# Kernel optimization log

Measured on AMD Instinct MI355X. Metric: run time of the kernel, lower is better.

The kernel has to match this reference:

```python
import jax, jax.numpy as jnp
import numpy as np

N = 100000   # nodes
E = 1600000  # directed edges (avg degree 16)
IN = 256     # input feature dim


def _gcn_norm(src, dst, n):
    # PyG gcn_norm with unit edge weights: deg computed on destination,
    # norm = deg^{-1/2}[src] * deg^{-1/2}[dst]
    deg = jax.ops.segment_sum(jnp.ones_like(dst, jnp.float32), dst, num_segments=n)
    dinv = jnp.where(deg > 0, jax.lax.rsqrt(deg), 0.0)
    return dinv[src] * dinv[dst]


def _gcn_conv(x, W, b, src, dst, norm, n):
    h = x @ W                          # [N, out] dense transform first (PyG order)
    msg = norm[:, None] * h[src]       # gather + scale  [E+N, out]
    agg = jax.ops.segment_sum(msg, dst, num_segments=n)  # scatter-add
    return agg + b


def setup_inputs() -> dict:
    key = jax.random.key(0)
    ks = jax.random.split(key, 5)
    x = jax.random.normal(ks[0], (N, IN), jnp.float32)
    edge_index = jax.random.randint(ks[1], (2, E), 0, N, dtype=jnp.int32)
    W1 = jax.random.normal(ks[2], (IN, 64), jnp.float32) * (1.0 / np.sqrt(IN))
    b1 = jnp.zeros((64,), jnp.float32)
    W2 = jax.random.normal(ks[3], (64, 32), jnp.float32) * (1.0 / np.sqrt(64))
    b2 = jnp.zeros((32,), jnp.float32)
    Wlin = jax.random.normal(ks[4], (32, 1), jnp.float32) * (1.0 / np.sqrt(32))
    blin = jnp.zeros((1,), jnp.float32)
    return {"x": x, "edge_index": edge_index, "W1": W1, "b1": b1,
            "W2": W2, "b2": b2, "Wlin": Wlin, "blin": blin}


def reference(x, edge_index, W1, b1, W2, b2, Wlin, blin):
    n = x.shape[0]
    loops = jnp.arange(n, dtype=edge_index.dtype)  # add self-loops (GCNConv default)
    src = jnp.concatenate([edge_index[0], loops])
    dst = jnp.concatenate([edge_index[1], loops])
    norm = _gcn_norm(src, dst, n)                  # same for both layers
    h = jax.nn.relu(_gcn_conv(x, W1, b1, src, dst, norm, n))
    h = jax.nn.relu(_gcn_conv(h, W2, b2, src, dst, norm, n))
    return h @ Wlin + blin
```

## Files before the change

### kernel.cpp

```cpp
#include <hip/hip_runtime.h>
#include <hip/hip_fp16.h>
#include <math.h>


#define BSH  9
#define BCAP 12288

typedef _Float16 half8 __attribute__((ext_vector_type(8)));
typedef _Float16 half4 __attribute__((ext_vector_type(4)));
typedef float floatx4 __attribute__((ext_vector_type(4)));

#define XT_STRIDE 40

static __global__ __launch_bounds__(256) void k_wfrag(const float* __restrict__ W1,
                                                      _Float16* __restrict__ w1f,
                                                      int* __restrict__ bkt_cnt) {
    int t = threadIdx.x;
    bkt_cnt[t] = 0;
    for (int idx = t; idx < 2048; idx += 256) {
        int kb = idx >> 8;
        int nt = (idx >> 6) & 3;
        int l  = idx & 63;
        int k0 = kb * 32 + ((l >> 4) << 3);
        int nn = nt * 16 + (l & 15);
        half8 b;
        #pragma unroll
        for (int j = 0; j < 8; ++j) b[j] = (_Float16)W1[(k0 + j) * 64 + nn];
        *(half8*)(w1f + (size_t)idx * 8) = b;
    }
}

static __global__ __launch_bounds__(256) void k_fat(const float* __restrict__ x,
                                                    const _Float16* __restrict__ w1f,
                                                    _Float16* __restrict__ h1f,
                                                    const int* __restrict__ src,
                                                    const int* __restrict__ dst,
                                                    int* __restrict__ bkt_cnt,
                                                    int* __restrict__ epack,
                                                    int n, int e, int nScat) {
    __shared__ alignas(16) char smem[32768 + 2 * 128 * XT_STRIDE * 2];
    int t = threadIdx.x;

    if ((int)blockIdx.x < nScat) {
        int*           sp    = (int*)smem;
        unsigned char* sbkt  = (unsigned char*)(smem + 16384);
        int*           cnt   = (int*)(smem + 20480);
        int*           loff  = (int*)(smem + 21504);
        int*           lcur  = (int*)(smem + 22528);
        int*           gbase = (int*)(smem + 23552);
        int*           sh    = (int*)(smem + 24576);
        int cb = blockIdx.x * 4096;
        int cc = min(4096, e - cb);

        cnt[t] = 0;
        __syncthreads();
        int ep[16]; unsigned char eb[16];
        int nv = 0;
        #pragma unroll
        for (int k = 0; k < 16; ++k) {
            int i = cb + k * 256 + t;
            if (i < e) {
                int s = src[i], d = dst[i];
                int b = d >> BSH;
                ep[nv] = ((d & 511) << 17) | s;
                eb[nv] = (unsigned char)b;
                atomicAdd(&cnt[b], 1);
                ++nv;
            }
        }
        __syncthreads();
        int v = cnt[t];
        sh[t] = v;
        __syncthreads();
        for (int o = 1; o < 256; o <<= 1) {
            int u = (t >= o) ? sh[t - o] : 0;
            __syncthreads();
            sh[t] += u;
            __syncthreads();
        }
        loff[t] = sh[t] - v;
        lcur[t] = sh[t] - v;
        if (v > 0) gbase[t] = t * BCAP + atomicAdd(&bkt_cnt[t], v);
        __syncthreads();
        for (int k = 0; k < nv; ++k) {
            int b = eb[k];
            int p = atomicAdd(&lcur[b], 1);
            sp[p] = ep[k];
            sbkt[p] = (unsigned char)b;
        }
        __syncthreads();
        for (int i = t; i < cc; i += 256) {
            int b = sbkt[i];
            epack[gbase[b] + (i - loff[b])] = sp[i];
        }
    } else {
        _Float16* Wl = (_Float16*)smem;
        _Float16* xt = (_Float16*)(smem + 32768);
        {
            const float4* s = (const float4*)w1f;
            float4* d = (float4*)smem;
            #pragma unroll
            for (int i = 0; i < 8; ++i) d[t + i * 256] = s[t + i * 256];
        }

        int l = t & 63;
        int w = t >> 6;
        int r0 = (blockIdx.x - nScat) * 128;
        int kq = (l >> 4) << 3;
        int lrow0 = w * 32 + (l & 15);
        int lrow1 = lrow0 + 16;

        int srow[4], sc4[4];
        const float* sgp[4];
        #pragma unroll
        for (int i = 0; i < 4; ++i) {
            int f = t + i * 256;
            srow[i] = f >> 3;
            sc4[i]  = f & 7;
            int gr  = r0 + srow[i];
            gr = gr < n ? gr : n - 1;
            sgp[i] = x + (size_t)gr * 256 + sc4[i] * 4;
        }

        floatx4 acc[2][4];
        #pragma unroll
        for (int mt = 0; mt < 2; ++mt)
            #pragma unroll
            for (int nt = 0; nt < 4; ++nt)
                acc[mt][nt] = (floatx4){0.f, 0.f, 0.f, 0.f};

        float4 pre[4];
        #pragma unroll
        for (int i = 0; i < 4; ++i) pre[i] = *(const float4*)(sgp[i]);
        #pragma unroll
        for (int i = 0; i < 4; ++i) {
            half4 h;
            h[0] = (_Float16)pre[i].x; h[1] = (_Float16)pre[i].y;
            h[2] = (_Float16)pre[i].z; h[3] = (_Float16)pre[i].w;
            *(half4*)(xt + srow[i] * XT_STRIDE + sc4[i] * 4) = h;
        }
        __syncthreads();

        #pragma unroll
        for (int kb = 0; kb < 8; ++kb) {
            if (kb < 7) {
                #pragma unroll
                for (int i = 0; i < 4; ++i)
                    pre[i] = *(const float4*)(sgp[i] + (kb + 1) * 32);
            }
            const _Float16* cur = xt + (kb & 1) * (128 * XT_STRIDE);
            half8 a0 = *(const half8*)(cur + lrow0 * XT_STRIDE + kq);
            half8 a1 = *(const half8*)(cur + lrow1 * XT_STRIDE + kq);
            #pragma unroll
            for (int nt = 0; nt < 4; ++nt) {
                half8 b = *(const half8*)(Wl + ((size_t)(kb * 4 + nt) * 64 + l) * 8);
                acc[0][nt] = __builtin_amdgcn_mfma_f32_16x16x32_f16(a0, b, acc[0][nt], 0, 0, 0);
                acc[1][nt] = __builtin_amdgcn_mfma_f32_16x16x32_f16(a1, b, acc[1][nt], 0, 0, 0);
            }
            if (kb < 7) {
                _Float16* nxt = xt + ((kb + 1) & 1) * (128 * XT_STRIDE);
                #pragma unroll
                for (int i = 0; i < 4; ++i) {
                    half4 h;
                    h[0] = (_Float16)pre[i].x; h[1] = (_Float16)pre[i].y;
                    h[2] = (_Float16)pre[i].z; h[3] = (_Float16)pre[i].w;
                    *(half4*)(nxt + srow[i] * XT_STRIDE + sc4[i] * 4) = h;
                }
                __syncthreads();
            }
        }

        int quad = l >> 4;
        int col  = l & 15;
        int rb0  = r0 + w * 32;
        #pragma unroll
        for (int mt = 0; mt < 2; ++mt) {
            #pragma unroll
            for (int r = 0; r < 4; ++r) {
                int rr = rb0 + mt * 16 + quad * 4 + r;
                if (rr < n) {
                    _Float16* o = h1f + (size_t)rr * 64 + col;
                    #pragma unroll
                    for (int nt = 0; nt < 4; ++nt)
                        o[nt * 16] = (_Float16)acc[mt][nt][r];
                }
            }
        }
    }
}

static __global__ __launch_bounds__(512) void k_bfinal(const int* __restrict__ bkt_cnt,
                                                       const int* __restrict__ epack,
                                                       float* __restrict__ dinv,
                                                       int* __restrict__ offs,
                                                       int* __restrict__ csr_src, int n) {
    __shared__ int cnt[512], sh[512], lcur[512];
    int t = threadIdx.x;
    int base = blockIdx.x << BSH;
    int e0 = blockIdx.x * BCAP;
    int e1 = e0 + bkt_cnt[blockIdx.x];
    cnt[t] = 0;
    __syncthreads();
    for (int i = e0 + t; i < e1; i += 512) atomicAdd(&cnt[epack[i] >> 17], 1);
    __syncthreads();
    int v = cnt[t];
    if (base + t < n) dinv[base + t] = 1.0f / sqrtf((float)(v + 1));
    sh[t] = v;
    __syncthreads();
    for (int o = 1; o < 512; o <<= 1) {
        int u = (t >= o) ? sh[t - o] : 0;
        __syncthreads();
        sh[t] += u;
        __syncthreads();
    }
    int incl = sh[t];
    if (base + t < n) offs[base + t] = e0 + incl;
    lcur[t] = e0 + incl - v;
    __syncthreads();
    for (int i = e0 + t; i < e1; i += 512) {
        int p = epack[i];
        int d = p >> 17;
        int pos = atomicAdd(&lcur[d], 1);
        csr_src[pos] = p & 0x1FFFF;
    }
}

static __global__ __launch_bounds__(512) void k_wpack(int* __restrict__ csr_src,
                                                      const float* __restrict__ dinv,
                                                      const int* __restrict__ bkt_cnt) {
    int b  = blockIdx.x;
    int e0 = b * BCAP;
    int e1 = e0 + bkt_cnt[b];
    for (int i = e0 + threadIdx.x; i < e1; i += 512) {
        int s = csr_src[i];
        int q = (int)(dinv[s] * 32767.0f + 0.5f);
        csr_src[i] = s | (q << 17);
    }
}

static __global__ __launch_bounds__(256) void k_agg1gemm2(const int* __restrict__ offs,
                                                          const int* __restrict__ csr_src,
                                                          const float* __restrict__ dinv,
                                                          const uint2* __restrict__ h1q,
                                                          const float* __restrict__ b1,
                                                          const float* __restrict__ W2,
                                                          __half2* __restrict__ h2h, int n) {
    __shared__ float Wl[64 * 32];
    __shared__ float aggL[16][64];
    int t = threadIdx.x;
    *(float4*)(Wl + t * 4)        = *(const float4*)(W2 + t * 4);
    *(float4*)(Wl + t * 4 + 1024) = *(const float4*)(W2 + t * 4 + 1024);

    int li = t & 15;
    int ni = t >> 4;
    int node  = blockIdx.x * 16 + ni;
    int nodeC = node < n ? node : n - 1;
    int start = (nodeC & 511) ? offs[nodeC - 1] : (nodeC >> BSH) * BCAP;
    int end   = offs[nodeC];
    float dd  = dinv[nodeC];

    uint2 su = h1q[(size_t)nodeC * 16 + li];
    float2 s01 = __half22float2(*(const __half2*)&su.x);
    float2 s23 = __half22float2(*(const __half2*)&su.y);
    float a0 = dd * s01.x, a1 = dd * s01.y, a2 = dd * s23.x, a3 = dd * s23.y;

    const float QS = 1.0f / 32767.0f;
    int j = start;
    for (; j + 7 < end; j += 8) {
        int pk[8];
        #pragma unroll
        for (int u = 0; u < 8; ++u) pk[u] = csr_src[j + u];
        uint2 vv[8]; float wq[8];
        #pragma unroll
        for (int u = 0; u < 8; ++u) {
            int s = pk[u] & 0x1FFFF;
            wq[u] = (float)(((unsigned)pk[u]) >> 17) * QS;
            vv[u] = h1q[(size_t)s * 16 + li];
        }
        #pragma unroll
        for (int u = 0; u < 8; ++u) {
            float2 v01 = __half22float2(*(const __half2*)&vv[u].x);
            float2 v23 = __half22float2(*(const __half2*)&vv[u].y);
            a0 += wq[u] * v01.x; a1 += wq[u] * v01.y;
            a2 += wq[u] * v23.x; a3 += wq[u] * v23.y;
        }
    }
    for (; j < end; ++j) {
        int p = csr_src[j];
        int s = p & 0x1FFFF;
        float wv = (float)(((unsigned)p) >> 17) * QS;
        uint2 v = h1q[(size_t)s * 16 + li];
        float2 v01 = __half22float2(*(const __half2*)&v.x);
        float2 v23 = __half22float2(*(const __half2*)&v.y);
        a0 += wv * v01.x; a1 += wv * v01.y;
        a2 += wv * v23.x; a3 += wv * v23.y;
    }
    float4 bb = *(const float4*)(b1 + li * 4);
    aggL[ni][li * 4 + 0] = fmaxf(dd * a0 + bb.x, 0.f);
    aggL[ni][li * 4 + 1] = fmaxf(dd * a1 + bb.y, 0.f);
    aggL[ni][li * 4 + 2] = fmaxf(dd * a2 + bb.z, 0.f);
    aggL[ni][li * 4 + 3] = fmaxf(dd * a3 + bb.w, 0.f);
    __syncthreads();

    if (node < n) {
        float s0 = 0.f, s1 = 0.f;
        #pragma unroll
        for (int k = 0; k < 64; ++k) {
            float a = aggL[ni][k];
            float2 wv = *(const float2*)(Wl + k * 32 + li * 2);
            s0 += a * wv.x;
            s1 += a * wv.y;
        }
        h2h[(size_t)node * 16 + li] = __float22half2_rn(make_float2(s0, s1));
    }
}

static __global__ __launch_bounds__(256) void k_gather2f(const int* __restrict__ offs,
                                                         const int* __restrict__ csr_src,
                                                         const float* __restrict__ dinv,
                                                         const uint2* __restrict__ h2q,
                                                         const float* __restrict__ b2,
                                                         const float* __restrict__ Wlin,
                                                         const float* __restrict__ blin,
                                                         float* __restrict__ out, int n) {
    int g    = blockIdx.x * 256 + threadIdx.x;
    int node = g >> 3;
    if (node >= n) return;
    int li = g & 7;
    int start = (node & 511) ? offs[node - 1] : (node >> BSH) * BCAP;
    int end   = offs[node];
    float dd  = dinv[node];

    uint2 su = h2q[(size_t)node * 8 + li];
    float2 s01 = __half22float2(*(const __half2*)&su.x);
    float2 s23 = __half22float2(*(const __half2*)&su.y);
    float a0 = dd * s01.x, a1 = dd * s01.y, a2 = dd * s23.x, a3 = dd * s23.y;

    const float QS = 1.0f / 32767.0f;
    int j = start;
    for (; j + 7 < end; j += 8) {
        int pk[8];
        #pragma unroll
        for (int u = 0; u < 8; ++u) pk[u] = csr_src[j + u];
        uint2 vv[8]; float wq[8];
        #pragma unroll
        for (int u = 0; u < 8; ++u) {
            int s = pk[u] & 0x1FFFF;
            wq[u] = (float)(((unsigned)pk[u]) >> 17) * QS;
            vv[u] = h2q[(size_t)s * 8 + li];
        }
        #pragma unroll
        for (int u = 0; u < 8; ++u) {
            float2 v01 = __half22float2(*(const __half2*)&vv[u].x);
            float2 v23 = __half22float2(*(const __half2*)&vv[u].y);
            a0 += wq[u] * v01.x; a1 += wq[u] * v01.y;
            a2 += wq[u] * v23.x; a3 += wq[u] * v23.y;
        }
    }
    for (; j < end; ++j) {
        int p = csr_src[j];
        int s = p & 0x1FFFF;
        float wv = (float)(((unsigned)p) >> 17) * QS;
        uint2 v = h2q[(size_t)s * 8 + li];
        float2 v01 = __half22float2(*(const __half2*)&v.x);
        float2 v23 = __half22float2(*(const __half2*)&v.y);
        a0 += wv * v01.x; a1 += wv * v01.y;
        a2 += wv * v23.x; a3 += wv * v23.y;
    }
    float4 bb = *(const float4*)(b2 + li * 4);
    float4 wl = *(const float4*)(Wlin + li * 4);
    float val = fmaxf(dd * a0 + bb.x, 0.f) * wl.x +
                fmaxf(dd * a1 + bb.y, 0.f) * wl.y +
                fmaxf(dd * a2 + bb.z, 0.f) * wl.z +
                fmaxf(dd * a3 + bb.w, 0.f) * wl.w;
    val += __shfl_xor(val, 4);
    val += __shfl_xor(val, 2);
    val += __shfl_xor(val, 1);
    if (li == 0) out[node] = val + blin[0];
}

extern "C" void kernel_launch(void* const* d_in, const int* in_sizes, int n_in,
                              void* d_out, int out_size, void* d_ws, size_t ws_size,
                              hipStream_t stream) {
    const float* x    = (const float*)d_in[0];
    const int*   ei   = (const int*)d_in[1];
    const float* W1   = (const float*)d_in[2];
    const float* b1   = (const float*)d_in[3];
    const float* W2   = (const float*)d_in[4];
    const float* b2   = (const float*)d_in[5];
    const float* Wlin = (const float*)d_in[6];
    const float* blin = (const float*)d_in[7];
    float* out = (float*)d_out;

    const int n = in_sizes[0] / 256;
    const int e = in_sizes[1] / 2;
    const int* src = ei;
    const int* dst = ei + e;
    const int nbkt  = (n + (1 << BSH) - 1) >> BSH;
    const int nScat = (e + 4095) / 4096;
    const int nGemm = (n + 127) / 128;

    char* wp = (char*)d_ws;
    _Float16* h1f = (_Float16*)wp;
    uint2*    h1q = (uint2*)wp;       wp += (size_t)n * 32 * 4;
    __half2*  h2h = (__half2*)wp;
    uint2*    h2q = (uint2*)wp;       wp += (size_t)n * 32 * 2;
    float*    dinv = (float*)wp;      wp += (size_t)n * 4;
    int*      offs = (int*)wp;        wp += (size_t)n * 4;
    int*      csr_src = (int*)wp;     wp += (size_t)nbkt * BCAP * 4;
    int*      epack = (int*)wp;       wp += (size_t)nbkt * BCAP * 4;
    int*      bkt_cnt = (int*)wp;     wp += 256 * 4;
    _Float16* w1f = (_Float16*)wp;

    dim3 B(256);
    k_wfrag <<<1, B, 0, stream>>>(W1, w1f, bkt_cnt);
    k_fat   <<<nScat + nGemm, B, 0, stream>>>(x, w1f, h1f, src, dst, bkt_cnt, epack, n, e, nScat);
    k_bfinal<<<nbkt, 512, 0, stream>>>(bkt_cnt, epack, dinv, offs, csr_src, n);
    k_wpack <<<nbkt, 512, 0, stream>>>(csr_src, dinv, bkt_cnt);
    k_agg1gemm2<<<(n + 15) / 16, B, 0, stream>>>(offs, csr_src, dinv, h1q, b1, W2, h2h, n);
    k_gather2f <<<(n * 8 + 255) / 256, B, 0, stream>>>(offs, csr_src, dinv, h2q,
                                                       b2, Wlin, blin, out, n);
}
```

Before: 288.2 us.

## Fold dinv weight packing into bucket finalize via global degree atomics

Removes the separate k_wpack kernel. The scatter phase now counts per-node degree with global atomics on a zeroed deg array, so k_bfinal can compute each source's quantized dinv directly while writing CSR entries. The GEMM blocks also stop staging W1 fragments in LDS and read them from global memory, which shrinks shared memory use and may raise occupancy. The trade-off is 1.6M extra global atomics in the scatter phase, a random deg[s] gather in k_bfinal, and a wider zeroing launch.

```diff
diff --git a/kernel.cpp b/kernel.cpp
--- a/kernel.cpp
+++ b/kernel.cpp
@@ -14,19 +14,25 @@
 
 static __global__ __launch_bounds__(256) void k_wfrag(const float* __restrict__ W1,
                                                       _Float16* __restrict__ w1f,
-                                                      int* __restrict__ bkt_cnt) {
+                                                      int* __restrict__ bkt_cnt,
+                                                      int* __restrict__ deg, int n) {
     int t = threadIdx.x;
-    bkt_cnt[t] = 0;
-    for (int idx = t; idx < 2048; idx += 256) {
-        int kb = idx >> 8;
-        int nt = (idx >> 6) & 3;
-        int l  = idx & 63;
-        int k0 = kb * 32 + ((l >> 4) << 3);
-        int nn = nt * 16 + (l & 15);
-        half8 b;
-        #pragma unroll
-        for (int j = 0; j < 8; ++j) b[j] = (_Float16)W1[(k0 + j) * 64 + nn];
-        *(half8*)(w1f + (size_t)idx * 8) = b;
+    int i0 = blockIdx.x * 512 + t;
+    if (i0 < n) deg[i0] = 0;
+    if (i0 + 256 < n) deg[i0 + 256] = 0;
+    if (blockIdx.x == 0) {
+        bkt_cnt[t] = 0;
+        for (int idx = t; idx < 2048; idx += 256) {
+            int kb = idx >> 8;
+            int nt = (idx >> 6) & 3;
+            int l  = idx & 63;
+            int k0 = kb * 32 + ((l >> 4) << 3);
+            int nn = nt * 16 + (l & 15);
+            half8 b;
+            #pragma unroll
+            for (int j = 0; j < 8; ++j) b[j] = (_Float16)W1[(k0 + j) * 64 + nn];
+            *(half8*)(w1f + (size_t)idx * 8) = b;
+        }
     }
 }
 
@@ -37,8 +43,9 @@
                                                     const int* __restrict__ dst,
                                                     int* __restrict__ bkt_cnt,
                                                     int* __restrict__ epack,
+                                                    int* __restrict__ deg,
                                                     int n, int e, int nScat) {
-    __shared__ alignas(16) char smem[32768 + 2 * 128 * XT_STRIDE * 2];
+    __shared__ alignas(16) char smem[25600];
     int t = threadIdx.x;
 
     if ((int)blockIdx.x < nScat) {
@@ -62,6 +69,7 @@
             if (i < e) {
                 int s = src[i], d = dst[i];
                 int b = d >> BSH;
+                atomicAdd(&deg[d], 1);
                 ep[nv] = ((d & 511) << 17) | s;
                 eb[nv] = (unsigned char)b;
                 atomicAdd(&cnt[b], 1);
@@ -94,14 +102,7 @@
             epack[gbase[b] + (i - loff[b])] = sp[i];
         }
     } else {
-        _Float16* Wl = (_Float16*)smem;
-        _Float16* xt = (_Float16*)(smem + 32768);
-        {
-            const float4* s = (const float4*)w1f;
-            float4* d = (float4*)smem;
-            #pragma unroll
-            for (int i = 0; i < 8; ++i) d[t + i * 256] = s[t + i * 256];
-        }
+        _Float16* xt = (_Float16*)smem;
 
         int l = t & 63;
         int w = t >> 6;
@@ -153,7 +154,7 @@
             half8 a1 = *(const half8*)(cur + lrow1 * XT_STRIDE + kq);
             #pragma unroll
             for (int nt = 0; nt < 4; ++nt) {
-                half8 b = *(const half8*)(Wl + ((size_t)(kb * 4 + nt) * 64 + l) * 8);
+                half8 b = *(const half8*)(w1f + ((size_t)(kb * 4 + nt) * 64 + l) * 8);
                 acc[0][nt] = __builtin_amdgcn_mfma_f32_16x16x32_f16(a0, b, acc[0][nt], 0, 0, 0);
                 acc[1][nt] = __builtin_amdgcn_mfma_f32_16x16x32_f16(a1, b, acc[1][nt], 0, 0, 0);
             }
@@ -191,6 +192,7 @@
 
 static __global__ __launch_bounds__(512) void k_bfinal(const int* __restrict__ bkt_cnt,
                                                        const int* __restrict__ epack,
+                                                       const int* __restrict__ deg,
                                                        float* __restrict__ dinv,
                                                        int* __restrict__ offs,
                                                        int* __restrict__ csr_src, int n) {
@@ -219,22 +221,12 @@
     __syncthreads();
     for (int i = e0 + t; i < e1; i += 512) {
         int p = epack[i];
-        int d = p >> 17;
-        int pos = atomicAdd(&lcur[d], 1);
-        csr_src[pos] = p & 0x1FFFF;
-    }
-}
-
-static __global__ __launch_bounds__(512) void k_wpack(int* __restrict__ csr_src,
-                                                      const float* __restrict__ dinv,
-                                                      const int* __restrict__ bkt_cnt) {
-    int b  = blockIdx.x;
-    int e0 = b * BCAP;
-    int e1 = e0 + bkt_cnt[b];
-    for (int i = e0 + threadIdx.x; i < e1; i += 512) {
-        int s = csr_src[i];
-        int q = (int)(dinv[s] * 32767.0f + 0.5f);
-        csr_src[i] = s | (q << 17);
+        int dn = p >> 17;
+        int s = p & 0x1FFFF;
+        int pos = atomicAdd(&lcur[dn], 1);
+        float di = 1.0f / sqrtf((float)(deg[s] + 1));
+        int q = (int)(di * 32767.0f + 0.5f);
+        csr_src[pos] = s | (q << 17);
     }
 }
 
@@ -399,6 +391,7 @@
     const int nbkt  = (n + (1 << BSH) - 1) >> BSH;
     const int nScat = (e + 4095) / 4096;
     const int nGemm = (n + 127) / 128;
+    const int nZB   = (n + 511) / 512;
 
     char* wp = (char*)d_ws;
     _Float16* h1f = (_Float16*)wp;
@@ -410,13 +403,13 @@
     int*      csr_src = (int*)wp;     wp += (size_t)nbkt * BCAP * 4;
     int*      epack = (int*)wp;       wp += (size_t)nbkt * BCAP * 4;
     int*      bkt_cnt = (int*)wp;     wp += 256 * 4;
+    int*      deg = (int*)wp;         wp += (size_t)n * 4;
     _Float16* w1f = (_Float16*)wp;
 
     dim3 B(256);
-    k_wfrag <<<1, B, 0, stream>>>(W1, w1f, bkt_cnt);
-    k_fat   <<<nScat + nGemm, B, 0, stream>>>(x, w1f, h1f, src, dst, bkt_cnt, epack, n, e, nScat);
-    k_bfinal<<<nbkt, 512, 0, stream>>>(bkt_cnt, epack, dinv, offs, csr_src, n);
-    k_wpack <<<nbkt, 512, 0, stream>>>(csr_src, dinv, bkt_cnt);
+    k_wfrag <<<nZB, B, 0, stream>>>(W1, w1f, bkt_cnt, deg, n);
+    k_fat   <<<nScat + nGemm, B, 0, stream>>>(x, w1f, h1f, src, dst, bkt_cnt, epack, deg, n, e, nScat);
+    k_bfinal<<<nbkt, 512, 0, stream>>>(bkt_cnt, epack, deg, dinv, offs, csr_src, n);
     k_agg1gemm2<<<(n + 15) / 16, B, 0, stream>>>(offs, csr_src, dinv, h1q, b1, W2, h2h, n);
     k_gather2f <<<(n * 8 + 255) / 256, B, 0, stream>>>(offs, csr_src, dinv, h2q,
                                                        b2, Wlin, blin, out, n);
```

New measurement: 317.0 us. 1.1x slower.
